# Optimization experiments

Measured on AMD Instinct MI355X. Metric: run time of the kernel, lower is better.

The kernel has to match this reference:

```python
import jax, jax.numpy as jnp
import numpy as np

EMBED_DIM = 512
NUM_HEADS = 8
HEAD_DIM = EMBED_DIM // NUM_HEADS
SCALE = HEAD_DIM ** -0.5
B, N = 4, 2048


def setup_inputs() -> dict:
    key = jax.random.key(0)
    ks = jax.random.split(key, 6)
    x = jax.random.normal(ks[0], (B, N, EMBED_DIM), dtype=jnp.float32)
    mask = jnp.ones((B, N, N), dtype=jnp.int32)
    # nn.Linear params: weight [out, in], bias [out]
    lim_qkv = 1.0 / np.sqrt(EMBED_DIM)
    qkv_w = jax.random.uniform(ks[1], (3 * EMBED_DIM, EMBED_DIM), jnp.float32, -lim_qkv, lim_qkv)
    qkv_b = jax.random.uniform(ks[2], (3 * EMBED_DIM,), jnp.float32, -lim_qkv, lim_qkv)
    proj_w = jax.random.uniform(ks[3], (EMBED_DIM, EMBED_DIM), jnp.float32, -lim_qkv, lim_qkv)
    proj_b = jax.random.uniform(ks[4], (EMBED_DIM,), jnp.float32, -lim_qkv, lim_qkv)
    return {"x": x, "qkv_w": qkv_w, "qkv_b": qkv_b, "proj_w": proj_w, "proj_b": proj_b, "mask": mask}


def reference(x, qkv_w, qkv_b, proj_w, proj_b, mask):
    Bb, Nn, C = x.shape
    qkv = (jnp.einsum('bnc,oc->bno', x, qkv_w) + qkv_b).reshape(Bb, Nn, 3, NUM_HEADS, HEAD_DIM)
    qkv = jnp.transpose(qkv, (2, 0, 3, 1, 4))
    q, k, v = qkv[0], qkv[1], qkv[2]
    # full score matrix [B,H,N,N] (faithful to the unfused original)
    attn = jnp.einsum('bhnd,bhmd->bhnm', q, k) * SCALE
    attn = jnp.where(mask[:, None, :, :] == 0, -jnp.inf, attn)
    attn = jax.nn.softmax(attn, axis=-1)
    out = jnp.einsum('bhnm,bhmd->bhnd', attn, v)
    out = jnp.transpose(out, (0, 2, 1, 3)).reshape(Bb, Nn, C)
    out = jnp.einsum('bnc,oc->bno', out, proj_w) + proj_b
    return out
```

## Files before the change

kernel.cpp:

```cpp
#include <hip/hip_runtime.h>
#include <hip/hip_bf16.h>
#include <stdint.h>

#define NB 4
#define NH 8
#define SEQ 2048
#define HD 64
#define CDIM 512

using bf16 = __hip_bfloat16;
typedef __attribute__((ext_vector_type(8))) short short8;
typedef __attribute__((ext_vector_type(4))) short short4_t;
typedef __attribute__((ext_vector_type(4))) float f32x4;

#define NEG_BIG (-3.0e38f)
#define SOFT_C 0.18033688011112042f

__device__ __forceinline__ short bf16_bits(float x) {
  return __builtin_bit_cast(short, __float2bfloat16(x));
}

__device__ __forceinline__ void gld_lds16(const void* g, void* l) {
  __builtin_amdgcn_global_load_lds(
      (const __attribute__((address_space(1))) unsigned int*)g,
      (__attribute__((address_space(3))) unsigned int*)l, 16, 0, 0);
}

#define X4 1048576
#define Q4 196608
#define P4 65536
__global__ __launch_bounds__(256) void prep_cvt(const float* __restrict__ x,
                                                const float* __restrict__ wq,
                                                const float* __restrict__ wp,
                                                short* __restrict__ xb,
                                                short* __restrict__ wqb,
                                                short* __restrict__ wpb) {
  int idx = blockIdx.x * 256 + threadIdx.x;
  int stride = gridDim.x * 256;
  for (int i = idx; i < X4 + Q4 + P4; i += stride) {
    const float* src; short* dst; int off;
    if (i < X4)            { src = x;  dst = xb;  off = i; }
    else if (i < X4 + Q4)  { src = wq; dst = wqb; off = i - X4; }
    else                   { src = wp; dst = wpb; off = i - X4 - Q4; }
    f32x4 v = *(const f32x4*)(src + (size_t)off * 4);
    short4_t o;
    o[0] = bf16_bits(v[0]); o[1] = bf16_bits(v[1]);
    o[2] = bf16_bits(v[2]); o[3] = bf16_bits(v[3]);
    *(short4_t*)(dst + (size_t)off * 4) = o;
  }
}

__global__ __launch_bounds__(256) void qkv_union(const short* __restrict__ Xb,
                                                 const short* __restrict__ Wb,
                                                 const float* __restrict__ bias,
                                                 const int* __restrict__ mask,
                                                 unsigned long long* __restrict__ bits,
                                                 bf16* __restrict__ q,
                                                 bf16* __restrict__ k,
                                                 bf16* __restrict__ vt) {
  __shared__ short Alds[128][32];
  __shared__ short Blds[128][32];
  const int tid = threadIdx.x;
  const int lane = tid & 63;
  const int w = tid >> 6;

  if (blockIdx.x < 512) {
    int wave_g = blockIdx.x * 4 + w;
#pragma unroll 1
    for (int i = 0; i < 32; i++) {
      size_t c = (size_t)i * 2048 + wave_g;
      size_t base = c * 256;
      int v0 = mask[base + 0 * 64 + lane];
      int v1 = mask[base + 1 * 64 + lane];
      int v2 = mask[base + 2 * 64 + lane];
      int v3 = mask[base + 3 * 64 + lane];
      unsigned long long w0 = __ballot(v0 != 0);
      unsigned long long w1 = __ballot(v1 != 0);
      unsigned long long w2 = __ballot(v2 != 0);
      unsigned long long w3 = __ballot(v3 != 0);
      if (lane == 0) {
        bits[c * 4 + 0] = w0; bits[c * 4 + 1] = w1;
        bits[c * 4 + 2] = w2; bits[c * 4 + 3] = w3;
      }
    }
    return;
  }

  const int g = blockIdx.x - 512;
  const int wm = w >> 1, wn = w & 1;
  const int row0 = (g & 63) * 128;
  const int col0 = (g >> 6) * 128;
  const bool isv = (col0 >= 1024);

  f32x4 acc[4][4] = {};
  const int cl = lane & 15;
  const int quad = lane >> 4;

  const int st_r = lane >> 2;
  const int st_gc = (lane & 3) ^ (st_r & 3);
  const int st_col = st_gc * 8;
  const int fc = (quad ^ (cl & 3)) * 8;

  for (int kk = 0; kk < 512; kk += 32) {
#pragma unroll
    for (int t = 0; t < 2; t++) {
      int R = w * 32 + t * 16;
      gld_lds16(&Xb[(size_t)(row0 + R + st_r) * 512 + kk + st_col], &Alds[R][0]);
      gld_lds16(&Wb[(size_t)(col0 + R + st_r) * 512 + kk + st_col], &Blds[R][0]);
    }
    __syncthreads();
    short8 a[4], b[4];
#pragma unroll
    for (int i = 0; i < 4; i++) a[i] = *(const short8*)&Alds[wm * 64 + i * 16 + cl][fc];
#pragma unroll
    for (int j = 0; j < 4; j++) b[j] = *(const short8*)&Blds[wn * 64 + j * 16 + cl][fc];
    if (!isv) {
#pragma unroll
      for (int i = 0; i < 4; i++)
#pragma unroll
        for (int j = 0; j < 4; j++)
          acc[i][j] = __builtin_amdgcn_mfma_f32_16x16x32_bf16(a[i], b[j], acc[i][j], 0, 0, 0);
    } else {
#pragma unroll
      for (int i = 0; i < 4; i++)
#pragma unroll
        for (int j = 0; j < 4; j++)
          acc[i][j] = __builtin_amdgcn_mfma_f32_16x16x32_bf16(b[j], a[i], acc[i][j], 0, 0, 0);
    }
    __syncthreads();
  }

  if (!isv) {
#pragma unroll
    for (int i = 0; i < 4; i++) {
#pragma unroll
      for (int j = 0; j < 4; j++) {
        int col = col0 + wn * 64 + j * 16 + cl;
        float bv = bias[col];
        int which = col >> 9;
        int c = col & 511;
        int h = c >> 6, d = c & 63;
#pragma unroll
        for (int r = 0; r < 4; r++) {
          int row = row0 + wm * 64 + i * 16 + quad * 4 + r;
          int bb = row >> 11, n = row & 2047;
          float val = acc[i][j][r] + bv;
          size_t bh = (size_t)bb * NH + h;
          if (which == 0)      q[(bh * SEQ + n) * HD + d] = __float2bfloat16(val * SOFT_C);
          else                 k[(bh * SEQ + n) * HD + d] = __float2bfloat16(val);
        }
      }
    }
  } else {
#pragma unroll
    for (int i = 0; i < 4; i++) {
#pragma unroll
      for (int j = 0; j < 4; j++) {
        int nrow = row0 + wm * 64 + i * 16 + cl;
        int bb = nrow >> 11, n = nrow & 2047;
#pragma unroll
        for (int r = 0; r < 4; r++) {
          int col = col0 + wn * 64 + j * 16 + quad * 4 + r;
          float bv = bias[col];
          int c = col & 511;
          int h = c >> 6, d = c & 63;
          float val = acc[i][j][r] + bv;
          size_t bh = (size_t)bb * NH + h;
          vt[(bh * HD + d) * SEQ + n] = __float2bfloat16(val);
        }
      }
    }
  }
}

__global__ __launch_bounds__(256) void flash_attn(const bf16* __restrict__ qg,
                                                  const bf16* __restrict__ kg,
                                                  const bf16* __restrict__ vg,
                                                  const unsigned long long* __restrict__ mbits,
                                                  bf16* __restrict__ attn_out) {
  __shared__ short Klds[64][64];
  __shared__ short Vlds[64][64];
  __shared__ short Plds[4][16][72];
  __shared__ unsigned long long Mlds[128];

  const int tid = threadIdx.x;
  const int lane = tid & 63;
  const int w = tid >> 6;
  const int qt = blockIdx.x;
  const int h = blockIdx.y;
  const int b = blockIdx.z;

  const size_t bh = (size_t)b * NH + h;
  const bf16* qp = qg + bh * SEQ * HD;
  const bf16* kp = kg + bh * SEQ * HD;
  const bf16* vp = vg + bh * HD * SEQ;

  const int cl = lane & 15;
  const int quad = lane >> 4;
  const int koff = quad * 8;
  const int qrow_w = qt * 128 + w * 32;

  const int c0 = ((quad ^ (cl & 7)) * 8);

  const int st_row = lane >> 3;
  const int st_chunk = (lane & 7) ^ st_row;
  const int st_col = st_chunk * 8;

  short8 aq[2][2];
#pragma unroll
  for (int g = 0; g < 2; g++) {
    aq[g][0] = *(const short8*)&qp[(size_t)(qrow_w + g * 16 + cl) * HD + koff];
    aq[g][1] = *(const short8*)&qp[(size_t)(qrow_w + g * 16 + cl) * HD + 32 + koff];
  }

  f32x4 o[2][4] = {};
  float l_l[2] = {0.f, 0.f};

  for (int kt = 0; kt < 32; kt++) {
    const int kb = kt * 64;
#pragma unroll
    for (int t = 0; t < 2; t++) {
      int rbase = w * 16 + t * 8;
      gld_lds16(&kp[(size_t)(kb + rbase + st_row) * HD + st_col], &Klds[rbase][0]);
      gld_lds16(&vp[(size_t)(rbase + st_row) * SEQ + kb + st_col], &Vlds[rbase][0]);
    }
    if (tid < 128) Mlds[tid] = mbits[((size_t)b * SEQ + qt * 128 + tid) * (SEQ / 64) + kt];
    __syncthreads();

    short8 k0[4], k1[4], vb[2][4];
#pragma unroll
    for (int nb = 0; nb < 4; nb++) {
      k0[nb] = *(const short8*)&Klds[nb * 16 + cl][c0];
      k1[nb] = *(const short8*)&Klds[nb * 16 + cl][c0 ^ 32];
    }
#pragma unroll
    for (int ks = 0; ks < 2; ks++)
#pragma unroll
      for (int db = 0; db < 4; db++)
        vb[ks][db] = *(const short8*)&Vlds[db * 16 + cl][c0 ^ (ks * 32)];

#pragma unroll
    for (int g = 0; g < 2; g++) {
      f32x4 s[4];
#pragma unroll
      for (int nb = 0; nb < 4; nb++) {
        f32x4 z = {0.f, 0.f, 0.f, 0.f};
        z = __builtin_amdgcn_mfma_f32_16x16x32_bf16(k0[nb], aq[g][0], z, 0, 0, 0);
        s[nb] = __builtin_amdgcn_mfma_f32_16x16x32_bf16(k1[nb], aq[g][1], z, 0, 0, 0);
      }

      unsigned long long wd = Mlds[w * 32 + g * 16 + cl];
      if (wd != ~0ULL) {
#pragma unroll
        for (int nb = 0; nb < 4; nb++)
#pragma unroll
          for (int r = 0; r < 4; r++)
            if (!((wd >> (nb * 16 + quad * 4 + r)) & 1ULL)) s[nb][r] = NEG_BIG;
      }

      float ps = 0.f;
#pragma unroll
      for (int nb = 0; nb < 4; nb++)
#pragma unroll
        for (int r = 0; r < 4; r++) {
          float p = __builtin_amdgcn_exp2f(s[nb][r]);
          s[nb][r] = p;
          ps += p;
        }
      ps += __shfl_xor(ps, 16);
      ps += __shfl_xor(ps, 32);
      l_l[g] += ps;

#pragma unroll
      for (int nb = 0; nb < 4; nb++) {
        short4_t pk;
        pk[0] = bf16_bits(s[nb][0]); pk[1] = bf16_bits(s[nb][1]);
        pk[2] = bf16_bits(s[nb][2]); pk[3] = bf16_bits(s[nb][3]);
        *(short4_t*)&Plds[w][cl][nb * 16 + quad * 4] = pk;
      }

#pragma unroll
      for (int ks = 0; ks < 2; ks++) {
        short8 pa = *(const short8*)&Plds[w][cl][ks * 32 + koff];
#pragma unroll
        for (int db = 0; db < 4; db++)
          o[g][db] = __builtin_amdgcn_mfma_f32_16x16x32_bf16(pa, vb[ks][db], o[g][db], 0, 0, 0);
      }
    }
    __syncthreads();
  }

#pragma unroll
  for (int g = 0; g < 2; g++) {
    float inv = 1.0f / l_l[g];
#pragma unroll
    for (int r = 0; r < 4; r++) {
      float ir = __shfl(inv, (lane & 48) + quad * 4 + r);
      int row = qrow_w + g * 16 + quad * 4 + r;
#pragma unroll
      for (int db = 0; db < 4; db++) {
        float val = o[g][db][r] * ir;
        attn_out[((size_t)b * SEQ + row) * CDIM + h * 64 + db * 16 + cl] = __float2bfloat16(val);
      }
    }
  }
}

__global__ __launch_bounds__(256) void proj_gemm(const bf16* __restrict__ X,
                                                 const short* __restrict__ Wb,
                                                 const float* __restrict__ bias,
                                                 float* __restrict__ out) {
  __shared__ short Alds[128][32];
  __shared__ short Blds[128][32];
  const int tid = threadIdx.x;
  const int lane = tid & 63;
  const int w = tid >> 6;
  const int wm = w >> 1, wn = w & 1;
  const int row0 = blockIdx.x * 128;
  const int col0 = blockIdx.y * 128;

  f32x4 acc[4][4] = {};
  const int cl = lane & 15;
  const int quad = lane >> 4;

  const int st_r = lane >> 2;
  const int st_gc = (lane & 3) ^ (st_r & 3);
  const int st_col = st_gc * 8;
  const int fc = (quad ^ (cl & 3)) * 8;

  for (int kk = 0; kk < 512; kk += 32) {
#pragma unroll
    for (int t = 0; t < 2; t++) {
      int R = w * 32 + t * 16;
      gld_lds16(&X[(size_t)(row0 + R + st_r) * 512 + kk + st_col], &Alds[R][0]);
      gld_lds16(&Wb[(size_t)(col0 + R + st_r) * 512 + kk + st_col], &Blds[R][0]);
    }
    __syncthreads();
    short8 a[4], b[4];
#pragma unroll
    for (int i = 0; i < 4; i++) a[i] = *(const short8*)&Alds[wm * 64 + i * 16 + cl][fc];
#pragma unroll
    for (int j = 0; j < 4; j++) b[j] = *(const short8*)&Blds[wn * 64 + j * 16 + cl][fc];
#pragma unroll
    for (int i = 0; i < 4; i++)
#pragma unroll
      for (int j = 0; j < 4; j++)
        acc[i][j] = __builtin_amdgcn_mfma_f32_16x16x32_bf16(a[i], b[j], acc[i][j], 0, 0, 0);
    __syncthreads();
  }

#pragma unroll
  for (int i = 0; i < 4; i++) {
#pragma unroll
    for (int j = 0; j < 4; j++) {
      int col = col0 + wn * 64 + j * 16 + cl;
      float bv = bias[col];
#pragma unroll
      for (int r = 0; r < 4; r++) {
        int row = row0 + wm * 64 + i * 16 + quad * 4 + r;
        out[(size_t)row * 512 + col] = acc[i][j][r] + bv;
      }
    }
  }
}

extern "C" void kernel_launch(void* const* d_in, const int* in_sizes, int n_in,
                              void* d_out, int out_size, void* d_ws, size_t ws_size,
                              hipStream_t stream) {
  const float* x      = (const float*)d_in[0];
  const float* qkv_w  = (const float*)d_in[1];
  const float* qkv_b  = (const float*)d_in[2];
  const float* proj_w = (const float*)d_in[3];
  const float* proj_b = (const float*)d_in[4];
  const int*   mask   = (const int*)d_in[5];
  float* out = (float*)d_out;

  char* ws = (char*)d_ws;
  bf16* q    = (bf16*)(ws);
  bf16* k    = (bf16*)(ws + 8388608);
  bf16* vt   = (bf16*)(ws + 16777216);
  bf16* attn = (bf16*)(ws + 25165824);
  short* xb  = (short*)(ws + 25165824);
  unsigned long long* mbits = (unsigned long long*)(ws + 33554432);
  short* wqb = (short*)(ws + 35651584);
  short* wpb = (short*)(ws + 37224448);

  prep_cvt<<<dim3(1280), 256, 0, stream>>>(x, qkv_w, proj_w, xb, wqb, wpb);
  qkv_union<<<dim3(512 + 768), 256, 0, stream>>>(xb, wqb, qkv_b, mask, mbits, q, k, vt);
  flash_attn<<<dim3(SEQ / 128, NH, NB), 256, 0, stream>>>(q, k, vt, mbits, attn);
  proj_gemm<<<dim3(64, 4), 256, 0, stream>>>(attn, wpb, proj_b, out);
}
```

Measured before the change: 228.9 us.

## Double-buffer K/V/mask tiles in LDS and batch QK MFMAs across row groups

Measured after the change: 225.5 us. Within noise of the previous version (-1.5%).

```diff
diff --git a/kernel.cpp b/kernel.cpp
--- a/kernel.cpp
+++ b/kernel.cpp
@@ -178,10 +178,10 @@
                                                   const bf16* __restrict__ vg,
                                                   const unsigned long long* __restrict__ mbits,
                                                   bf16* __restrict__ attn_out) {
-  __shared__ short Klds[64][64];
-  __shared__ short Vlds[64][64];
-  __shared__ short Plds[4][16][72];
-  __shared__ unsigned long long Mlds[128];
+  __shared__ short Klds[2][64][64];
+  __shared__ short Vlds[2][64][64];
+  __shared__ short Plds[4][2][16][72];
+  __shared__ unsigned long long Mlds[2][128];
 
   const int tid = threadIdx.x;
   const int lane = tid & 63;
@@ -216,78 +216,92 @@
   f32x4 o[2][4] = {};
   float l_l[2] = {0.f, 0.f};
 
+#pragma unroll
+  for (int t = 0; t < 2; t++) {
+    int rbase = w * 16 + t * 8;
+    gld_lds16(&kp[(size_t)(rbase + st_row) * HD + st_col], &Klds[0][rbase][0]);
+    gld_lds16(&vp[(size_t)(rbase + st_row) * SEQ + st_col], &Vlds[0][rbase][0]);
+  }
+  if (tid < 128) Mlds[0][tid] = mbits[((size_t)b * SEQ + qt * 128 + tid) * (SEQ / 64) + 0];
+
   for (int kt = 0; kt < 32; kt++) {
-    const int kb = kt * 64;
-#pragma unroll
-    for (int t = 0; t < 2; t++) {
-      int rbase = w * 16 + t * 8;
-      gld_lds16(&kp[(size_t)(kb + rbase + st_row) * HD + st_col], &Klds[rbase][0]);
-      gld_lds16(&vp[(size_t)(rbase + st_row) * SEQ + kb + st_col], &Vlds[rbase][0]);
-    }
-    if (tid < 128) Mlds[tid] = mbits[((size_t)b * SEQ + qt * 128 + tid) * (SEQ / 64) + kt];
+    const int cur = kt & 1;
     __syncthreads();
 
+    if (kt + 1 < 32) {
+      const int kb2 = (kt + 1) * 64;
+#pragma unroll
+      for (int t = 0; t < 2; t++) {
+        int rbase = w * 16 + t * 8;
+        gld_lds16(&kp[(size_t)(kb2 + rbase + st_row) * HD + st_col], &Klds[cur ^ 1][rbase][0]);
+        gld_lds16(&vp[(size_t)(rbase + st_row) * SEQ + kb2 + st_col], &Vlds[cur ^ 1][rbase][0]);
+      }
+      if (tid < 128)
+        Mlds[cur ^ 1][tid] = mbits[((size_t)b * SEQ + qt * 128 + tid) * (SEQ / 64) + kt + 1];
+    }
+
     short8 k0[4], k1[4], vb[2][4];
 #pragma unroll
     for (int nb = 0; nb < 4; nb++) {
-      k0[nb] = *(const short8*)&Klds[nb * 16 + cl][c0];
-      k1[nb] = *(const short8*)&Klds[nb * 16 + cl][c0 ^ 32];
+      k0[nb] = *(const short8*)&Klds[cur][nb * 16 + cl][c0];
+      k1[nb] = *(const short8*)&Klds[cur][nb * 16 + cl][c0 ^ 32];
     }
 #pragma unroll
     for (int ks = 0; ks < 2; ks++)
 #pragma unroll
       for (int db = 0; db < 4; db++)
-        vb[ks][db] = *(const short8*)&Vlds[db * 16 + cl][c0 ^ (ks * 32)];
-
-#pragma unroll
-    for (int g = 0; g < 2; g++) {
-      f32x4 s[4];
+        vb[ks][db] = *(const short8*)&Vlds[cur][db * 16 + cl][c0 ^ (ks * 32)];
+
+    f32x4 s[2][4];
+#pragma unroll
+    for (int g = 0; g < 2; g++)
 #pragma unroll
       for (int nb = 0; nb < 4; nb++) {
         f32x4 z = {0.f, 0.f, 0.f, 0.f};
         z = __builtin_amdgcn_mfma_f32_16x16x32_bf16(k0[nb], aq[g][0], z, 0, 0, 0);
-        s[nb] = __builtin_amdgcn_mfma_f32_16x16x32_bf16(k1[nb], aq[g][1], z, 0, 0, 0);
-      }
-
-      unsigned long long wd = Mlds[w * 32 + g * 16 + cl];
+        s[g][nb] = __builtin_amdgcn_mfma_f32_16x16x32_bf16(k1[nb], aq[g][1], z, 0, 0, 0);
+      }
+
+#pragma unroll
+    for (int g = 0; g < 2; g++) {
+      unsigned long long wd = Mlds[cur][w * 32 + g * 16 + cl];
       if (wd != ~0ULL) {
 #pragma unroll
         for (int nb = 0; nb < 4; nb++)
 #pragma unroll
           for (int r = 0; r < 4; r++)
-            if (!((wd >> (nb * 16 + quad * 4 + r)) & 1ULL)) s[nb][r] = NEG_BIG;
-      }
-
+            if (!((wd >> (nb * 16 + quad * 4 + r)) & 1ULL)) s[g][nb][r] = NEG_BIG;
+      }
       float ps = 0.f;
 #pragma unroll
       for (int nb = 0; nb < 4; nb++)
 #pragma unroll
         for (int r = 0; r < 4; r++) {
-          float p = __builtin_amdgcn_exp2f(s[nb][r]);
-          s[nb][r] = p;
+          float p = __builtin_amdgcn_exp2f(s[g][nb][r]);
+          s[g][nb][r] = p;
           ps += p;
         }
       ps += __shfl_xor(ps, 16);
       ps += __shfl_xor(ps, 32);
       l_l[g] += ps;
-
 #pragma unroll
       for (int nb = 0; nb < 4; nb++) {
         short4_t pk;
-        pk[0] = bf16_bits(s[nb][0]); pk[1] = bf16_bits(s[nb][1]);
-        pk[2] = bf16_bits(s[nb][2]); pk[3] = bf16_bits(s[nb][3]);
-        *(short4_t*)&Plds[w][cl][nb * 16 + quad * 4] = pk;
-      }
-
+        pk[0] = bf16_bits(s[g][nb][0]); pk[1] = bf16_bits(s[g][nb][1]);
+        pk[2] = bf16_bits(s[g][nb][2]); pk[3] = bf16_bits(s[g][nb][3]);
+        *(short4_t*)&Plds[w][g][cl][nb * 16 + quad * 4] = pk;
+      }
+    }
+
+#pragma unroll
+    for (int g = 0; g < 2; g++)
 #pragma unroll
       for (int ks = 0; ks < 2; ks++) {
-        short8 pa = *(const short8*)&Plds[w][cl][ks * 32 + koff];
+        short8 pa = *(const short8*)&Plds[w][g][cl][ks * 32 + koff];
 #pragma unroll
         for (int db = 0; db < 4; db++)
           o[g][db] = __builtin_amdgcn_mfma_f32_16x16x32_bf16(pa, vb[ks][db], o[g][db], 0, 0, 0);
       }
-    }
-    __syncthreads();
   }
 
 #pragma unroll
```
